# Kernel tuning notes

Measured on AMD Instinct MI355X. Metric: run time of the kernel, lower is better.

Reference implementation:

```python
import jax, jax.numpy as jnp
import numpy as np

N, MAXDEG, D = 100000, 16, 128
HID, OUT, BLOCKS, NUM_GRAPHS = 256, 1, 5, 2048
BN_EPS = 1e-5


def setup_inputs() -> dict:
    key = jax.random.key(0)
    ks = jax.random.split(key, 10)
    s = 0.05  # small init scale for stability across 5 residual blocks
    x = jax.random.normal(ks[0], (N, D), jnp.float32)
    nbr = jax.random.randint(ks[1], (N, MAXDEG), 0, N)
    pad_mask = jax.random.uniform(ks[2], (N, MAXDEG)) < 0.2
    padded_neighbors = jnp.where(pad_mask, -1, nbr)
    membership = jnp.sort(jax.random.randint(ks[3], (N,), 0, NUM_GRAPHS))
    return dict(
        x=x,
        padded_neighbors=padded_neighbors,
        membership=membership,
        merge_W=jax.random.normal(ks[4], (BLOCKS, 2 * D, D), jnp.float32) * s,
        merge_b=jnp.zeros((BLOCKS, D), jnp.float32),
        lin1_W=jax.random.normal(ks[5], (BLOCKS, D, HID), jnp.float32) * s,
        lin1_b=jnp.zeros((BLOCKS, HID), jnp.float32),
        lin2_W=jax.random.normal(ks[6], (BLOCKS, HID, D), jnp.float32) * s,
        lin2_b=jnp.zeros((BLOCKS, D), jnp.float32),
        bn_g=jnp.ones((BLOCKS, D), jnp.float32),
        bn_b=jnp.zeros((BLOCKS, D), jnp.float32),
        eps=jnp.full((BLOCKS,), 0.1, jnp.float32),
        dense0_W=jax.random.normal(ks[7], (D * (BLOCKS + 1), HID), jnp.float32) * s,
        dense0_b=jnp.zeros((HID,), jnp.float32),
        dense1_W=jax.random.normal(ks[8], (HID, D), jnp.float32) * s,
        dense1_b=jnp.zeros((D,), jnp.float32),
        bn0_g=jnp.ones((D,), jnp.float32),
        bn0_b=jnp.zeros((D,), jnp.float32),
        dense2_W=jax.random.normal(ks[9], (D, OUT), jnp.float32) * s,
        dense2_b=jnp.zeros((OUT,), jnp.float32),
    )


def _bn(h, g, b):
    # BatchNorm1d in training mode: batch stats, biased variance
    m = h.mean(0)
    v = h.var(0)
    return g * (h - m) * jax.lax.rsqrt(v + BN_EPS) + b


def _forward(x, padded_neighbors, membership, merge_W, merge_b, lin1_W, lin1_b,
             lin2_W, lin2_b, bn_g, bn_b, eps, dense0_W, dense0_b, dense1_W,
             dense1_b, bn0_g, bn0_b, dense2_W, dense2_b):
    # map padding value -1 to dummy row index N (mirrors torch's x_with_dummy[-1])
    idx = jnp.where(padded_neighbors >= 0, padded_neighbors, N)  # (N, MAXDEG)
    h = x
    xs = [x]
    for i in range(BLOCKS):
        # 'sum' aggregation == spmm(unnormalized adj, h): padded gather + sum
        hw_sum = jnp.concatenate([h, jnp.zeros((1, D), h.dtype)], axis=0)
        s_aggr = hw_sum[idx].sum(axis=1)  # (N, D)
        hw_max = jnp.concatenate([h, h.min(axis=0, keepdims=True)], axis=0)
        m_aggr = hw_max[idx].max(axis=1)  # (N, D)
        # merge='cat' -> merge_layer
        z = jnp.concatenate([s_aggr, m_aggr], axis=1) @ merge_W[i] + merge_b[i]
        # self_connection + learned eps * x_org
        z = z + h + eps[i] * h
        # backbone: Linear->ReLU->Linear->ReLU->BatchNorm1d
        z = jax.nn.relu(z @ lin1_W[i] + lin1_b[i])
        z = jax.nn.relu(z @ lin2_W[i] + lin2_b[i])
        z = _bn(z, bn_g[i], bn_b[i])
        xs.append(z)
        h = h + z  # add_dense_connection=True
    cat = jnp.concatenate(xs, axis=1)  # (N, D*(BLOCKS+1))
    # readout_method='sum': graph-level scatter-sum over membership
    g = jax.ops.segment_sum(cat, membership, num_segments=NUM_GRAPHS)
    g = jax.nn.relu(g @ dense0_W + dense0_b)
    g = jax.nn.relu(g @ dense1_W + dense1_b)
    g = _bn(g, bn0_g, bn0_b)
    return g @ dense2_W + dense2_b  # (NUM_GRAPHS, OUT)


def reference(x, padded_neighbors, membership, merge_W, merge_b, lin1_W, lin1_b,
              lin2_W, lin2_b, bn_g, bn_b, eps, dense0_W, dense0_b, dense1_W,
              dense1_b, bn0_g, bn0_b, dense2_W, dense2_b):
    return _forward(x, padded_neighbors, membership, merge_W, merge_b, lin1_W,
                    lin1_b, lin2_W, lin2_b, bn_g, bn_b, eps, dense0_W, dense0_b,
                    dense1_W, dense1_b, bn0_g, bn0_b, dense2_W, dense2_b)
```

## Files before the change

kernel.cpp:

```cpp
#include <hip/hip_runtime.h>
#include <hip/hip_bf16.h>
#include <math.h>

#define N_NODES 100000
#define DD 128
#define MAXDEG 16
#define HIDW 256
#define NBLOCKS 5
#define NGRAPH 2048
#define CATW 768

typedef __attribute__((ext_vector_type(8))) short short8;
typedef __attribute__((ext_vector_type(4))) float f32x4;

__device__ __forceinline__ float b2f(ushort u) {
    union { unsigned int i; float f; } x; x.i = ((unsigned int)u) << 16; return x.f;
}
__device__ __forceinline__ ushort f2b(float f) {
    unsigned int x = __float_as_uint(f);
    unsigned int r = (x + 0x7fffu + ((x >> 16) & 1u)) >> 16;
    return (ushort)r;
}
__device__ __forceinline__ unsigned int encf(float f) {
    unsigned int b = __float_as_uint(f);
    return (b & 0x80000000u) ? ~b : (b | 0x80000000u);
}
__device__ __forceinline__ float decf(unsigned int e) {
    return __uint_as_float((e & 0x80000000u) ? (e & 0x7fffffffu) : ~e);
}

__global__ __launch_bounds__(256)
void k_init(const float* __restrict__ x, float* __restrict__ h, ushort* __restrict__ hb)
{
    size_t i = ((size_t)blockIdx.x * 256 + threadIdx.x) * 4;
    float4 v = *reinterpret_cast<const float4*>(x + i);
    *reinterpret_cast<float4*>(h + i) = v;
    ushort4 u;
    u.x = f2b(v.x); u.y = f2b(v.y); u.z = f2b(v.z); u.w = f2b(v.w);
    *reinterpret_cast<ushort4*>(hb + i) = u;
}

__global__ void k_setup(unsigned int* __restrict__ cmin, float* __restrict__ bnacc)
{
    int t = threadIdx.x;
    for (int i = t; i < 6 * DD; i += 256) cmin[i] = 0xFF800000u;
    for (int i = t; i < NBLOCKS * 2 * DD; i += 256) bnacc[i] = 0.f;
}

__global__ __launch_bounds__(256)
void k_convT(const float* __restrict__ src, ushort* __restrict__ dst, int K, int M, int total)
{
    int id = blockIdx.x * 256 + threadIdx.x;
    if (id >= total) return;
    int km = K * M;
    int b = id / km, rem = id - b * km;
    int m = rem / K, k = rem - m * K;
    dst[(size_t)b * km + (size_t)m * K + k] = f2b(src[(size_t)b * km + (size_t)k * M + m]);
}

__global__ __launch_bounds__(256)
void k_colmin_part(const float* __restrict__ h, float* __restrict__ part, int nrows)
{
    int t = threadIdx.x;
    int c = t & 127, half = t >> 7;
    int r0 = blockIdx.x * 256;
    int rend = r0 + 256; if (rend > nrows) rend = nrows;
    float m = INFINITY;
    for (int r = r0 + half; r < rend; r += 2)
        m = fminf(m, h[(size_t)r * DD + c]);
    __shared__ float sm[256];
    sm[t] = m;
    __syncthreads();
    if (half == 0) part[(size_t)blockIdx.x * DD + c] = fminf(sm[c], sm[c + 128]);
}

__global__ void k_colmin_fin(const float* __restrict__ part, unsigned int* __restrict__ colmin, int nb)
{
    int c = threadIdx.x;
    float m = INFINITY;
    for (int b = 0; b < nb; ++b) m = fminf(m, part[(size_t)b * DD + c]);
    colmin[c] = encf(m);
}

__global__ __launch_bounds__(256)
void k_aggregate_b(const ushort* __restrict__ hb, const int* __restrict__ nbr,
                   const unsigned int* __restrict__ cmin, ushort* __restrict__ A)
{
    int t = threadIdx.x;
    int node = blockIdx.x * 8 + (t >> 5);
    int c0 = (t & 31) * 4;
    const int* row = nbr + (size_t)node * MAXDEG;
    float s0 = 0.f, s1 = 0.f, s2 = 0.f, s3 = 0.f;
    float m0 = -INFINITY, m1 = -INFINITY, m2 = -INFINITY, m3 = -INFINITY;
    int cnt = 0;
#pragma unroll
    for (int j = 0; j < MAXDEG; ++j) {
        int id = row[j];
        if (id >= 0) {
            uint2 v = *reinterpret_cast<const uint2*>(hb + (size_t)id * DD + c0);
            float f0 = __uint_as_float(v.x << 16);
            float f1 = __uint_as_float(v.x & 0xffff0000u);
            float f2 = __uint_as_float(v.y << 16);
            float f3 = __uint_as_float(v.y & 0xffff0000u);
            s0 += f0; s1 += f1; s2 += f2; s3 += f3;
            m0 = fmaxf(m0, f0); m1 = fmaxf(m1, f1);
            m2 = fmaxf(m2, f2); m3 = fmaxf(m3, f3);
            ++cnt;
        }
    }
    if (cnt == 0) {
        m0 = decf(cmin[c0]); m1 = decf(cmin[c0 + 1]);
        m2 = decf(cmin[c0 + 2]); m3 = decf(cmin[c0 + 3]);
    }
    ushort4 us, um;
    us.x = f2b(s0); us.y = f2b(s1); us.z = f2b(s2); us.w = f2b(s3);
    um.x = f2b(m0); um.y = f2b(m1); um.z = f2b(m2); um.w = f2b(m3);
    *reinterpret_cast<ushort4*>(A + (size_t)node * (2 * DD) + c0) = us;
    *reinterpret_cast<ushort4*>(A + (size_t)node * (2 * DD) + DD + c0) = um;
}

__global__ __launch_bounds__(256, 2)
void k_fused_mlp(const ushort* __restrict__ Ag, const float* __restrict__ h,
                 const ushort* __restrict__ mW, const ushort* __restrict__ w1,
                 const ushort* __restrict__ w2, const float* __restrict__ mb,
                 const float* __restrict__ b1, const float* __restrict__ b2,
                 const float* __restrict__ eps_ptr, float* __restrict__ uf,
                 float* __restrict__ bnacc)
{
    __shared__ __align__(16) char pool[72 * 1024];
    char* As = pool;
    char* Bs = pool + 8 * 1024;
    char* Zs = pool + 24 * 1024;
    char* Ts = pool + 40 * 1024;
    float* s1 = reinterpret_cast<float*>(pool);
    float* s2 = reinterpret_cast<float*>(pool) + 128;

    const int t = threadIdx.x;
    const int lane = t & 63, wave = t >> 6;
    const int wr = wave >> 1, wc = wave & 1;
    const int lr = lane & 15;
    const int lkb = (lane >> 4) << 4;
    const int rb = blockIdx.x * 64;

    f32x4 acc[2][4];
#pragma unroll
    for (int m = 0; m < 2; ++m)
#pragma unroll
        for (int n = 0; n < 4; ++n) acc[m][n] = (f32x4)(0.f);

    for (int k0 = 0; k0 < 256; k0 += 64) {
#pragma unroll
        for (int p = 0; p < 2; ++p) {
            int idx = p * 256 + t, row = idx >> 3, ch = idx & 7;
            int gr = rb + row;
            short8 v = {};
            if (gr < N_NODES)
                v = *reinterpret_cast<const short8*>(Ag + (size_t)gr * 256 + k0 + ch * 8);
            int byte = (row << 7) | (ch << 4); byte ^= (row & 7) << 4;
            *reinterpret_cast<short8*>(As + byte) = v;
        }
#pragma unroll
        for (int p = 0; p < 4; ++p) {
            int idx = p * 256 + t, row = idx >> 3, ch = idx & 7;
            short8 v = *reinterpret_cast<const short8*>(mW + (size_t)row * 256 + k0 + ch * 8);
            int byte = (row << 7) | (ch << 4); byte ^= (row & 7) << 4;
            *reinterpret_cast<short8*>(Bs + byte) = v;
        }
        __syncthreads();
#pragma unroll
        for (int k32 = 0; k32 < 2; ++k32) {
            short8 af[2], bq[4];
#pragma unroll
            for (int m = 0; m < 2; ++m) {
                int row = wr * 32 + m * 16 + lr;
                int byte = (row << 7) | (k32 * 64 + lkb); byte ^= (row & 7) << 4;
                af[m] = *reinterpret_cast<const short8*>(As + byte);
            }
#pragma unroll
            for (int n = 0; n < 4; ++n) {
                int col = wc * 64 + n * 16 + lr;
                int byte = (col << 7) | (k32 * 64 + lkb); byte ^= (col & 7) << 4;
                bq[n] = *reinterpret_cast<const short8*>(Bs + byte);
            }
#pragma unroll
            for (int m = 0; m < 2; ++m)
#pragma unroll
                for (int n = 0; n < 4; ++n)
                    acc[m][n] = __builtin_amdgcn_mfma_f32_16x16x32_bf16(af[m], bq[n], acc[m][n], 0, 0, 0);
        }
        __syncthreads();
    }
    {
        float alpha = 1.f + *eps_ptr;
#pragma unroll
        for (int m = 0; m < 2; ++m)
#pragma unroll
            for (int j = 0; j < 4; ++j) {
                int lrow = wr * 32 + m * 16 + (lane >> 4) * 4 + j;
                int grow = rb + lrow;
#pragma unroll
                for (int n = 0; n < 4; ++n) {
                    int col = wc * 64 + n * 16 + lr;
                    float z = acc[m][n][j] + mb[col];
                    if (grow < N_NODES) z += alpha * h[(size_t)grow * DD + col];
                    int byte = (lrow << 8) | (col << 1); byte ^= (lrow & 7) << 4;
                    *reinterpret_cast<ushort*>(Zs + byte) = f2b(z);
                }
            }
    }
    __syncthreads();

    f32x4 acb[2][8];
#pragma unroll
    for (int m = 0; m < 2; ++m)
#pragma unroll
        for (int n = 0; n < 8; ++n) acb[m][n] = (f32x4)(0.f);

    for (int kc = 0; kc < 4; ++kc) {
#pragma unroll
        for (int p = 0; p < 4; ++p) {
            int idx = p * 256 + t, row = idx >> 2, ch = idx & 3;
            short8 v = *reinterpret_cast<const short8*>(w1 + (size_t)row * 128 + kc * 32 + ch * 8);
            int byte = (row << 6) | (ch << 4); byte ^= (row & 3) << 4;
            *reinterpret_cast<short8*>(Bs + byte) = v;
        }
        __syncthreads();
        short8 af[2];
#pragma unroll
        for (int m = 0; m < 2; ++m) {
            int row = wr * 32 + m * 16 + lr;
            int byte = (row << 8) | (kc * 64 + lkb); byte ^= (row & 7) << 4;
            af[m] = *reinterpret_cast<const short8*>(Zs + byte);
        }
#pragma unroll
        for (int nh = 0; nh < 2; ++nh) {
            short8 bq[4];
#pragma unroll
            for (int q = 0; q < 4; ++q) {
                int wrow = wc * 128 + nh * 64 + q * 16 + lr;
                int byte = (wrow << 6) | lkb; byte ^= (wrow & 3) << 4;
                bq[q] = *reinterpret_cast<const short8*>(Bs + byte);
            }
#pragma unroll
            for (int m = 0; m < 2; ++m)
#pragma unroll
                for (int q = 0; q < 4; ++q)
                    acb[m][nh * 4 + q] = __builtin_amdgcn_mfma_f32_16x16x32_bf16(af[m], bq[q], acb[m][nh * 4 + q], 0, 0, 0);
        }
        __syncthreads();
    }
    {
#pragma unroll
        for (int m = 0; m < 2; ++m)
#pragma unroll
            for (int j = 0; j < 4; ++j) {
                int lrow = wr * 32 + m * 16 + (lane >> 4) * 4 + j;
#pragma unroll
                for (int nn = 0; nn < 8; ++nn) {
                    int col = wc * 128 + nn * 16 + lr;
                    float tv = fmaxf(acb[m][nn][j] + b1[col], 0.f);
                    int byte = (lrow << 9) | (col << 1); byte ^= (lrow & 7) << 4;
                    *reinterpret_cast<ushort*>(Ts + byte) = f2b(tv);
                }
            }
    }
    __syncthreads();

    f32x4 acu[2][4];
#pragma unroll
    for (int m = 0; m < 2; ++m)
#pragma unroll
        for (int n = 0; n < 4; ++n) acu[m][n] = (f32x4)(0.f);

    for (int k0 = 0; k0 < 256; k0 += 64) {
#pragma unroll
        for (int p = 0; p < 4; ++p) {
            int idx = p * 256 + t, row = idx >> 3, ch = idx & 7;
            short8 v = *reinterpret_cast<const short8*>(w2 + (size_t)row * 256 + k0 + ch * 8);
            int byte = (row << 7) | (ch << 4); byte ^= (row & 7) << 4;
            *reinterpret_cast<short8*>(Bs + byte) = v;
        }
        __syncthreads();
#pragma unroll
        for (int k32 = 0; k32 < 2; ++k32) {
            short8 af[2], bq[4];
#pragma unroll
            for (int m = 0; m < 2; ++m) {
                int row = wr * 32 + m * 16 + lr;
                int byte = (row << 9) | (k0 * 2 + k32 * 64 + lkb); byte ^= (row & 7) << 4;
                af[m] = *reinterpret_cast<const short8*>(Ts + byte);
            }
#pragma unroll
            for (int n = 0; n < 4; ++n) {
                int wrow = wc * 64 + n * 16 + lr;
                int byte = (wrow << 7) | (k32 * 64 + lkb); byte ^= (wrow & 7) << 4;
                bq[n] = *reinterpret_cast<const short8*>(Bs + byte);
            }
#pragma unroll
            for (int m = 0; m < 2; ++m)
#pragma unroll
                for (int n = 0; n < 4; ++n)
                    acu[m][n] = __builtin_amdgcn_mfma_f32_16x16x32_bf16(af[m], bq[n], acu[m][n], 0, 0, 0);
        }
        __syncthreads();
    }
    if (t < 128) { s1[t] = 0.f; s2[t] = 0.f; }
    __syncthreads();
    {
        float e1[4] = {0.f, 0.f, 0.f, 0.f}, e2[4] = {0.f, 0.f, 0.f, 0.f};
#pragma unroll
        for (int m = 0; m < 2; ++m)
#pragma unroll
            for (int j = 0; j < 4; ++j) {
                int grow = rb + wr * 32 + m * 16 + (lane >> 4) * 4 + j;
                if (grow >= N_NODES) continue;
#pragma unroll
                for (int n = 0; n < 4; ++n) {
                    int col = wc * 64 + n * 16 + lr;
                    float u = fmaxf(acu[m][n][j] + b2[col], 0.f);
                    uf[(size_t)grow * DD + col] = u;
                    e1[n] += u; e2[n] += u * u;
                }
            }
#pragma unroll
        for (int n = 0; n < 4; ++n) {
            int col = wc * 64 + n * 16 + lr;
            atomicAdd(&s1[col], e1[n]);
            atomicAdd(&s2[col], e2[n]);
        }
    }
    __syncthreads();
    if (t < 128) {
        atomicAdd(&bnacc[t], s1[t]);
        atomicAdd(&bnacc[128 + t], s2[t]);
    }
}

__global__ void k_bn_fin(const float* __restrict__ part, int nb, float inv_n,
                         float* __restrict__ mean, float* __restrict__ inv)
{
    int c = threadIdx.x;
    float s1 = 0.f, s2 = 0.f;
    for (int b = 0; b < nb; ++b) {
        s1 += part[(size_t)b * 256 + c];
        s2 += part[(size_t)b * 256 + 128 + c];
    }
    float m = s1 * inv_n;
    float v = s2 * inv_n - m * m;
    mean[c] = m;
    inv[c] = rsqrtf(v + 1e-5f);
}

__global__ __launch_bounds__(256)
void k_bn_apply_scan(const float* __restrict__ u, float* __restrict__ h,
                     ushort* __restrict__ hb,
                     const float* __restrict__ mean, const float* __restrict__ inv,
                     const float* __restrict__ gam, const float* __restrict__ bet,
                     const int* __restrict__ mem, float* __restrict__ G,
                     unsigned int* __restrict__ cmin_next,
                     int colbase, int nrows)
{
    int t = threadIdx.x;
    int c = t & 127, half = t >> 7;
    int r0 = blockIdx.x * 128;
    int rend = r0 + 128; if (rend > nrows) rend = nrows;
    float mu = mean[c], iv = inv[c], g = gam[c], b = bet[c];
    float accv = 0.f, lmin = INFINITY;
    int curg = -1;
    for (int r = r0 + half; r < rend; r += 2) {
        float z = g * (u[(size_t)r * DD + c] - mu) * iv + b;
        float hn = h[(size_t)r * DD + c] + z;
        h[(size_t)r * DD + c] = hn;
        hb[(size_t)r * DD + c] = f2b(hn);
        lmin = fminf(lmin, hn);
        int gg = mem[r];
        if (gg != curg) {
            if (curg >= 0) atomicAdd(&G[(size_t)curg * CATW + colbase + c], accv);
            curg = gg; accv = 0.f;
        }
        accv += z;
    }
    if (curg >= 0) atomicAdd(&G[(size_t)curg * CATW + colbase + c], accv);
    __shared__ float sm[256];
    sm[t] = lmin;
    __syncthreads();
    if (half == 0) atomicMin(&cmin_next[c], encf(fminf(sm[c], sm[c + 128])));
}

__global__ __launch_bounds__(256)
void k_scan_x(const float* __restrict__ x, const int* __restrict__ mem,
              float* __restrict__ G, int nrows)
{
    int t = threadIdx.x;
    int c = t & 127, half = t >> 7;
    int r0 = blockIdx.x * 128;
    int rend = r0 + 128; if (rend > nrows) rend = nrows;
    float accv = 0.f;
    int curg = -1;
    for (int r = r0 + half; r < rend; r += 2) {
        float z = x[(size_t)r * DD + c];
        int gg = mem[r];
        if (gg != curg) {
            if (curg >= 0) atomicAdd(&G[(size_t)curg * CATW + c], accv);
            curg = gg; accv = 0.f;
        }
        accv += z;
    }
    if (curg >= 0) atomicAdd(&G[(size_t)curg * CATW + c], accv);
}

__global__ __launch_bounds__(256)
void k_bn_part(const float* __restrict__ u, float* __restrict__ part, int nrows)
{
    int t = threadIdx.x;
    int c = t & 127, half = t >> 7;
    int r0 = blockIdx.x * 256;
    int rend = r0 + 256; if (rend > nrows) rend = nrows;
    float s1 = 0.f, s2 = 0.f;
    for (int r = r0 + half; r < rend; r += 2) {
        float v = u[(size_t)r * DD + c];
        s1 += v; s2 += v * v;
    }
    __shared__ float sh1[256], sh2[256];
    sh1[t] = s1; sh2[t] = s2;
    __syncthreads();
    if (half == 0) {
        part[(size_t)blockIdx.x * 256 + c]       = sh1[c] + sh1[c + 128];
        part[(size_t)blockIdx.x * 256 + 128 + c] = sh2[c] + sh2[c + 128];
    }
}

__global__ __launch_bounds__(256)
void k_read0(const float* __restrict__ G, const float* __restrict__ W,
             const float* __restrict__ b, float* __restrict__ o)
{
    __shared__ float As[8][CATW];
    int t = threadIdx.x;
    int rb = blockIdx.x * 8;
#pragma unroll
    for (int p = 0; p < 6; ++p) {
        int idx = p * 256 + t;
        int r = idx / 192, k4 = idx - r * 192;
        float4 v = *reinterpret_cast<const float4*>(G + (size_t)(rb + r) * CATW + k4 * 4);
        *reinterpret_cast<float4*>(&As[r][k4 * 4]) = v;
    }
    __syncthreads();
    float acc[8] = {0.f, 0.f, 0.f, 0.f, 0.f, 0.f, 0.f, 0.f};
    for (int k = 0; k < CATW; k += 4) {
        float w0 = W[(size_t)(k + 0) * HIDW + t];
        float w1 = W[(size_t)(k + 1) * HIDW + t];
        float w2 = W[(size_t)(k + 2) * HIDW + t];
        float w3 = W[(size_t)(k + 3) * HIDW + t];
#pragma unroll
        for (int r = 0; r < 8; ++r) {
            float4 a = *reinterpret_cast<const float4*>(&As[r][k]);
            acc[r] += a.x * w0 + a.y * w1 + a.z * w2 + a.w * w3;
        }
    }
    float bb = b[t];
#pragma unroll
    for (int r = 0; r < 8; ++r)
        o[(size_t)(rb + r) * HIDW + t] = fmaxf(acc[r] + bb, 0.f);
}

__global__ __launch_bounds__(256)
void k_read1(const float* __restrict__ A, const float* __restrict__ W,
             const float* __restrict__ b, float* __restrict__ o)
{
    __shared__ float As[16][HIDW];
    int t = threadIdx.x;
    int c = t & 127, rh = t >> 7;
    int rb = blockIdx.x * 16;
#pragma unroll
    for (int p = 0; p < 4; ++p) {
        int idx = p * 256 + t;
        int r = idx >> 6, k4 = idx & 63;
        float4 v = *reinterpret_cast<const float4*>(A + (size_t)(rb + r) * HIDW + k4 * 4);
        *reinterpret_cast<float4*>(&As[r][k4 * 4]) = v;
    }
    __syncthreads();
    float acc[8] = {0.f, 0.f, 0.f, 0.f, 0.f, 0.f, 0.f, 0.f};
    for (int k = 0; k < HIDW; k += 4) {
        float w0 = W[(size_t)(k + 0) * DD + c];
        float w1 = W[(size_t)(k + 1) * DD + c];
        float w2 = W[(size_t)(k + 2) * DD + c];
        float w3 = W[(size_t)(k + 3) * DD + c];
#pragma unroll
        for (int r = 0; r < 8; ++r) {
            float4 a = *reinterpret_cast<const float4*>(&As[rh * 8 + r][k]);
            acc[r] += a.x * w0 + a.y * w1 + a.z * w2 + a.w * w3;
        }
    }
    float bb = b[c];
#pragma unroll
    for (int r = 0; r < 8; ++r)
        o[(size_t)(rb + rh * 8 + r) * DD + c] = fmaxf(acc[r] + bb, 0.f);
}

__global__ __launch_bounds__(256)
void k_final(const float* __restrict__ g1, const float* __restrict__ mean,
             const float* __restrict__ inv, const float* __restrict__ gam,
             const float* __restrict__ bet, const float* __restrict__ W2,
             const float* __restrict__ b2, float* __restrict__ out)
{
    int w = threadIdx.x >> 6, lane = threadIdx.x & 63;
    int row = blockIdx.x * 4 + w;
    float s = 0.f;
#pragma unroll
    for (int q = 0; q < 2; ++q) {
        int c = lane + q * 64;
        float v = gam[c] * (g1[(size_t)row * DD + c] - mean[c]) * inv[c] + bet[c];
        s += v * W2[c];
    }
#pragma unroll
    for (int off = 32; off > 0; off >>= 1) s += __shfl_down(s, off);
    if (lane == 0) out[row] = s + b2[0];
}

extern "C" void kernel_launch(void* const* d_in, const int* in_sizes, int n_in,
                              void* d_out, int out_size, void* d_ws, size_t ws_size,
                              hipStream_t stream)
{
    const float* x       = (const float*)d_in[0];
    const int*   nbr     = (const int*)d_in[1];
    const int*   mem     = (const int*)d_in[2];
    const float* merge_W = (const float*)d_in[3];
    const float* merge_b = (const float*)d_in[4];
    const float* lin1_W  = (const float*)d_in[5];
    const float* lin1_b  = (const float*)d_in[6];
    const float* lin2_W  = (const float*)d_in[7];
    const float* lin2_b  = (const float*)d_in[8];
    const float* bn_g    = (const float*)d_in[9];
    const float* bn_b    = (const float*)d_in[10];
    const float* epsv    = (const float*)d_in[11];
    const float* d0W     = (const float*)d_in[12];
    const float* d0b     = (const float*)d_in[13];
    const float* d1W     = (const float*)d_in[14];
    const float* d1b     = (const float*)d_in[15];
    const float* bn0g    = (const float*)d_in[16];
    const float* bn0b    = (const float*)d_in[17];
    const float* d2W     = (const float*)d_in[18];
    const float* d2b     = (const float*)d_in[19];
    float* out = (float*)d_out;

    char* p = (char*)d_ws;
    auto alloc = [&](size_t bytes) { char* r = p; p += (bytes + 255) & ~(size_t)255; return r; };
    float*  h     = (float*)alloc((size_t)N_NODES * DD * 4);
    ushort* hb    = (ushort*)alloc((size_t)N_NODES * DD * 2);
    ushort* Abuf  = (ushort*)alloc((size_t)N_NODES * 2 * DD * 2);
    float*  uf    = (float*)alloc((size_t)N_NODES * DD * 4);
    float*  G     = (float*)alloc((size_t)NGRAPH * CATW * 4);
    float*  g0    = (float*)alloc((size_t)NGRAPH * HIDW * 4);
    float*  g1    = (float*)alloc((size_t)NGRAPH * DD * 4);
    float*  part  = (float*)alloc((size_t)391 * 256 * 4);
    float*  red   = (float*)alloc(1024 * 4);
    unsigned int* cminb = (unsigned int*)alloc(6 * DD * 4);
    float*  bnacc = (float*)alloc((size_t)NBLOCKS * 2 * DD * 4);
    ushort* mergeT = (ushort*)alloc((size_t)NBLOCKS * 2 * DD * DD * 2);
    ushort* lin1T  = (ushort*)alloc((size_t)NBLOCKS * DD * HIDW * 2);
    ushort* lin2T  = (ushort*)alloc((size_t)NBLOCKS * HIDW * DD * 2);
    float* meanp  = red + DD;
    float* invp   = red + 2 * DD;

    const int NBP = 391;
    const int NRB = 782;
    const int NFB = 1563;

    k_init<<<12500, 256, 0, stream>>>(x, h, hb);
    k_setup<<<1, 256, 0, stream>>>(cminb, bnacc);
    {
        int tm = NBLOCKS * 2 * DD * DD;
        k_convT<<<(tm + 255) / 256, 256, 0, stream>>>(merge_W, mergeT, 2 * DD, DD, tm);
        int t1 = NBLOCKS * DD * HIDW;
        k_convT<<<(t1 + 255) / 256, 256, 0, stream>>>(lin1_W, lin1T, DD, HIDW, t1);
        int t2 = NBLOCKS * HIDW * DD;
        k_convT<<<(t2 + 255) / 256, 256, 0, stream>>>(lin2_W, lin2T, HIDW, DD, t2);
    }
    hipMemsetAsync(G, 0, (size_t)NGRAPH * CATW * sizeof(float), stream);
    k_colmin_part<<<NBP, 256, 0, stream>>>(x, part, N_NODES);
    k_colmin_fin<<<1, 128, 0, stream>>>(part, cminb, NBP);
    k_scan_x<<<NRB, 256, 0, stream>>>(x, mem, G, N_NODES);

    for (int i = 0; i < NBLOCKS; ++i) {
        k_aggregate_b<<<N_NODES / 8, 256, 0, stream>>>(hb, nbr, cminb + (size_t)i * DD, Abuf);
        k_fused_mlp<<<NFB, 256, 0, stream>>>(
            Abuf, h,
            mergeT + (size_t)i * 2 * DD * DD,
            lin1T + (size_t)i * DD * HIDW,
            lin2T + (size_t)i * HIDW * DD,
            merge_b + (size_t)i * DD, lin1_b + (size_t)i * HIDW, lin2_b + (size_t)i * DD,
            epsv + i, uf, bnacc + (size_t)i * 2 * DD);
        k_bn_fin<<<1, 128, 0, stream>>>(bnacc + (size_t)i * 2 * DD, 1, 1.f / (float)N_NODES, meanp, invp);
        k_bn_apply_scan<<<NRB, 256, 0, stream>>>(uf, h, hb, meanp, invp,
                                                 bn_g + (size_t)i * DD, bn_b + (size_t)i * DD,
                                                 mem, G, cminb + (size_t)(i + 1) * DD,
                                                 (i + 1) * DD, N_NODES);
    }

    k_read0<<<NGRAPH / 8, 256, 0, stream>>>(G, d0W, d0b, g0);
    k_read1<<<NGRAPH / 16, 256, 0, stream>>>(g0, d1W, d1b, g1);
    k_bn_part<<<8, 256, 0, stream>>>(g1, part, NGRAPH);
    k_bn_fin<<<1, 128, 0, stream>>>(part, 8, 1.f / (float)NGRAPH, meanp, invp);
    k_final<<<NGRAPH / 4, 256, 0, stream>>>(g1, meanp, invp, bn0g, bn0b, d2W, d2b, out);
}
```

Baseline: 1.617 ms.

## Restructure fused MLP to per-wave row tiles with direct global weight fragments

Replaces the block-cooperative fused MLP, which staged A and weight tiles through LDS with many __syncthreads, with a kernel where each wave owns 32 rows. Each wave loads MFMA operand fragments for A and weights straight from global memory, using L2 for weight reuse. The hidden layer is processed in 32-column chunks so lin1 output feeds lin2 through a small per-wave LDS buffer without block barriers. BN statistics are reduced with wave shuffles before global atomics, and the aggregate kernel is widened to 8 columns per thread with 16-byte loads. The risk is higher global and L2 traffic for weights, since they are no longer shared across waves through LDS.

```diff
diff --git a/kernel.cpp b/kernel.cpp
--- a/kernel.cpp
+++ b/kernel.cpp
@@ -87,252 +87,193 @@
                    const unsigned int* __restrict__ cmin, ushort* __restrict__ A)
 {
     int t = threadIdx.x;
-    int node = blockIdx.x * 8 + (t >> 5);
-    int c0 = (t & 31) * 4;
+    int node = blockIdx.x * 16 + (t >> 4);
+    int c0 = (t & 15) * 8;
     const int* row = nbr + (size_t)node * MAXDEG;
-    float s0 = 0.f, s1 = 0.f, s2 = 0.f, s3 = 0.f;
-    float m0 = -INFINITY, m1 = -INFINITY, m2 = -INFINITY, m3 = -INFINITY;
+    float s[8], mx[8];
+#pragma unroll
+    for (int q = 0; q < 8; ++q) { s[q] = 0.f; mx[q] = -INFINITY; }
     int cnt = 0;
 #pragma unroll
     for (int j = 0; j < MAXDEG; ++j) {
         int id = row[j];
         if (id >= 0) {
-            uint2 v = *reinterpret_cast<const uint2*>(hb + (size_t)id * DD + c0);
-            float f0 = __uint_as_float(v.x << 16);
-            float f1 = __uint_as_float(v.x & 0xffff0000u);
-            float f2 = __uint_as_float(v.y << 16);
-            float f3 = __uint_as_float(v.y & 0xffff0000u);
-            s0 += f0; s1 += f1; s2 += f2; s3 += f3;
-            m0 = fmaxf(m0, f0); m1 = fmaxf(m1, f1);
-            m2 = fmaxf(m2, f2); m3 = fmaxf(m3, f3);
+            uint4 v = *reinterpret_cast<const uint4*>(hb + (size_t)id * DD + c0);
+            unsigned int w0 = v.x, w1 = v.y, w2 = v.z, w3 = v.w;
+            float f0 = __uint_as_float(w0 << 16),  f1 = __uint_as_float(w0 & 0xffff0000u);
+            float f2 = __uint_as_float(w1 << 16),  f3 = __uint_as_float(w1 & 0xffff0000u);
+            float f4 = __uint_as_float(w2 << 16),  f5 = __uint_as_float(w2 & 0xffff0000u);
+            float f6 = __uint_as_float(w3 << 16),  f7 = __uint_as_float(w3 & 0xffff0000u);
+            s[0] += f0; s[1] += f1; s[2] += f2; s[3] += f3;
+            s[4] += f4; s[5] += f5; s[6] += f6; s[7] += f7;
+            mx[0] = fmaxf(mx[0], f0); mx[1] = fmaxf(mx[1], f1);
+            mx[2] = fmaxf(mx[2], f2); mx[3] = fmaxf(mx[3], f3);
+            mx[4] = fmaxf(mx[4], f4); mx[5] = fmaxf(mx[5], f5);
+            mx[6] = fmaxf(mx[6], f6); mx[7] = fmaxf(mx[7], f7);
             ++cnt;
         }
     }
     if (cnt == 0) {
-        m0 = decf(cmin[c0]); m1 = decf(cmin[c0 + 1]);
-        m2 = decf(cmin[c0 + 2]); m3 = decf(cmin[c0 + 3]);
-    }
-    ushort4 us, um;
-    us.x = f2b(s0); us.y = f2b(s1); us.z = f2b(s2); us.w = f2b(s3);
-    um.x = f2b(m0); um.y = f2b(m1); um.z = f2b(m2); um.w = f2b(m3);
-    *reinterpret_cast<ushort4*>(A + (size_t)node * (2 * DD) + c0) = us;
-    *reinterpret_cast<ushort4*>(A + (size_t)node * (2 * DD) + DD + c0) = um;
-}
-
-__global__ __launch_bounds__(256, 2)
-void k_fused_mlp(const ushort* __restrict__ Ag, const float* __restrict__ h,
-                 const ushort* __restrict__ mW, const ushort* __restrict__ w1,
-                 const ushort* __restrict__ w2, const float* __restrict__ mb,
-                 const float* __restrict__ b1, const float* __restrict__ b2,
-                 const float* __restrict__ eps_ptr, float* __restrict__ uf,
-                 float* __restrict__ bnacc)
-{
-    __shared__ __align__(16) char pool[72 * 1024];
-    char* As = pool;
-    char* Bs = pool + 8 * 1024;
-    char* Zs = pool + 24 * 1024;
-    char* Ts = pool + 40 * 1024;
-    float* s1 = reinterpret_cast<float*>(pool);
-    float* s2 = reinterpret_cast<float*>(pool) + 128;
-
+#pragma unroll
+        for (int q = 0; q < 8; ++q) mx[q] = decf(cmin[c0 + q]);
+    }
+    short8 vs, vm;
+#pragma unroll
+    for (int q = 0; q < 8; ++q) { vs[q] = (short)f2b(s[q]); vm[q] = (short)f2b(mx[q]); }
+    *reinterpret_cast<short8*>(A + (size_t)node * (2 * DD) + c0) = vs;
+    *reinterpret_cast<short8*>(A + (size_t)node * (2 * DD) + DD + c0) = vm;
+}
+
+__global__ __launch_bounds__(256)
+void k_fused_wave(const ushort* __restrict__ Ag, const float* __restrict__ h,
+                  const ushort* __restrict__ mW, const ushort* __restrict__ w1,
+                  const ushort* __restrict__ w2, const float* __restrict__ mb,
+                  const float* __restrict__ b1, const float* __restrict__ b2,
+                  const float* __restrict__ eps_ptr, float* __restrict__ uf,
+                  float* __restrict__ bnacc)
+{
+    __shared__ __align__(16) char pool[40960];
     const int t = threadIdx.x;
     const int lane = t & 63, wave = t >> 6;
-    const int wr = wave >> 1, wc = wave & 1;
+    char* zs = pool + wave * 10240;
+    char* ts = zs + 8192;
     const int lr = lane & 15;
-    const int lkb = (lane >> 4) << 4;
-    const int rb = blockIdx.x * 64;
-
-    f32x4 acc[2][4];
+    const int lg = lane >> 4;
+    const int r0 = blockIdx.x * 128 + wave * 32;
+    const float alpha = 1.f + *eps_ptr;
+
+    f32x4 acc[2][8];
 #pragma unroll
     for (int m = 0; m < 2; ++m)
 #pragma unroll
-        for (int n = 0; n < 4; ++n) acc[m][n] = (f32x4)(0.f);
-
-    for (int k0 = 0; k0 < 256; k0 += 64) {
-#pragma unroll
-        for (int p = 0; p < 2; ++p) {
-            int idx = p * 256 + t, row = idx >> 3, ch = idx & 7;
-            int gr = rb + row;
-            short8 v = {};
-            if (gr < N_NODES)
-                v = *reinterpret_cast<const short8*>(Ag + (size_t)gr * 256 + k0 + ch * 8);
-            int byte = (row << 7) | (ch << 4); byte ^= (row & 7) << 4;
-            *reinterpret_cast<short8*>(As + byte) = v;
-        }
-#pragma unroll
-        for (int p = 0; p < 4; ++p) {
-            int idx = p * 256 + t, row = idx >> 3, ch = idx & 7;
-            short8 v = *reinterpret_cast<const short8*>(mW + (size_t)row * 256 + k0 + ch * 8);
-            int byte = (row << 7) | (ch << 4); byte ^= (row & 7) << 4;
-            *reinterpret_cast<short8*>(Bs + byte) = v;
-        }
-        __syncthreads();
-#pragma unroll
-        for (int k32 = 0; k32 < 2; ++k32) {
-            short8 af[2], bq[4];
+        for (int n = 0; n < 8; ++n) acc[m][n] = (f32x4)(0.f);
+
+    const ushort* agp = Ag + (size_t)(r0 + lr) * 256 + lg * 8;
+    const ushort* mwp = mW + (size_t)lr * 256 + lg * 8;
+    const bool ok0 = (r0 + lr) < N_NODES;
+    const bool ok1 = (r0 + 16 + lr) < N_NODES;
+#pragma unroll 2
+    for (int k32 = 0; k32 < 8; ++k32) {
+        short8 af0 = {}, af1 = {};
+        if (ok0) af0 = *reinterpret_cast<const short8*>(agp + k32 * 32);
+        if (ok1) af1 = *reinterpret_cast<const short8*>(agp + 16 * 256 + k32 * 32);
+#pragma unroll
+        for (int n = 0; n < 8; ++n) {
+            short8 bq = *reinterpret_cast<const short8*>(mwp + (size_t)n * 16 * 256 + k32 * 32);
+            acc[0][n] = __builtin_amdgcn_mfma_f32_16x16x32_bf16(af0, bq, acc[0][n], 0, 0, 0);
+            acc[1][n] = __builtin_amdgcn_mfma_f32_16x16x32_bf16(af1, bq, acc[1][n], 0, 0, 0);
+        }
+    }
+#pragma unroll
+    for (int m = 0; m < 2; ++m)
+#pragma unroll
+        for (int j = 0; j < 4; ++j) {
+            int lrow = m * 16 + lg * 4 + j;
+            int grow = r0 + lrow;
+#pragma unroll
+            for (int n = 0; n < 8; ++n) {
+                int col = n * 16 + lr;
+                float z = acc[m][n][j] + mb[col];
+                if (grow < N_NODES) z += alpha * h[(size_t)grow * DD + col];
+                int byte = (lrow << 8) | (col << 1);
+                byte ^= (lrow & 7) << 4;
+                *reinterpret_cast<ushort*>(zs + byte) = f2b(z);
+            }
+        }
+    asm volatile("s_waitcnt lgkmcnt(0)" ::: "memory");
+    __builtin_amdgcn_sched_barrier(0);
+
+    f32x4 au[2][8];
+#pragma unroll
+    for (int m = 0; m < 2; ++m)
+#pragma unroll
+        for (int n = 0; n < 8; ++n) au[m][n] = (f32x4)(0.f);
+
+    const ushort* w1p = w1 + (size_t)lr * 128 + lg * 8;
+    const ushort* w2p = w2 + (size_t)lr * 256 + lg * 8;
+    for (int hc = 0; hc < 8; ++hc) {
+        f32x4 at[2][2];
+#pragma unroll
+        for (int m = 0; m < 2; ++m)
+#pragma unroll
+            for (int n2 = 0; n2 < 2; ++n2) at[m][n2] = (f32x4)(0.f);
+#pragma unroll
+        for (int k32 = 0; k32 < 4; ++k32) {
+            short8 az[2];
 #pragma unroll
             for (int m = 0; m < 2; ++m) {
-                int row = wr * 32 + m * 16 + lr;
-                int byte = (row << 7) | (k32 * 64 + lkb); byte ^= (row & 7) << 4;
-                af[m] = *reinterpret_cast<const short8*>(As + byte);
+                int row = m * 16 + lr;
+                int byte = (row << 8) | (k32 << 6) | (lg << 4);
+                byte ^= (lr & 7) << 4;
+                az[m] = *reinterpret_cast<const short8*>(zs + byte);
             }
 #pragma unroll
-            for (int n = 0; n < 4; ++n) {
-                int col = wc * 64 + n * 16 + lr;
-                int byte = (col << 7) | (k32 * 64 + lkb); byte ^= (col & 7) << 4;
-                bq[n] = *reinterpret_cast<const short8*>(Bs + byte);
+            for (int n2 = 0; n2 < 2; ++n2) {
+                short8 bq = *reinterpret_cast<const short8*>(
+                    w1p + (size_t)(hc * 32 + n2 * 16) * 128 + k32 * 32);
+                at[0][n2] = __builtin_amdgcn_mfma_f32_16x16x32_bf16(az[0], bq, at[0][n2], 0, 0, 0);
+                at[1][n2] = __builtin_amdgcn_mfma_f32_16x16x32_bf16(az[1], bq, at[1][n2], 0, 0, 0);
             }
-#pragma unroll
-            for (int m = 0; m < 2; ++m)
-#pragma unroll
-                for (int n = 0; n < 4; ++n)
-                    acc[m][n] = __builtin_amdgcn_mfma_f32_16x16x32_bf16(af[m], bq[n], acc[m][n], 0, 0, 0);
-        }
-        __syncthreads();
-    }
-    {
-        float alpha = 1.f + *eps_ptr;
+        }
 #pragma unroll
         for (int m = 0; m < 2; ++m)
 #pragma unroll
             for (int j = 0; j < 4; ++j) {
-                int lrow = wr * 32 + m * 16 + (lane >> 4) * 4 + j;
-                int grow = rb + lrow;
-#pragma unroll
-                for (int n = 0; n < 4; ++n) {
-                    int col = wc * 64 + n * 16 + lr;
-                    float z = acc[m][n][j] + mb[col];
-                    if (grow < N_NODES) z += alpha * h[(size_t)grow * DD + col];
-                    int byte = (lrow << 8) | (col << 1); byte ^= (lrow & 7) << 4;
-                    *reinterpret_cast<ushort*>(Zs + byte) = f2b(z);
+                int lrow = m * 16 + lg * 4 + j;
+#pragma unroll
+                for (int n2 = 0; n2 < 2; ++n2) {
+                    int hcol = n2 * 16 + lr;
+                    float tv = fmaxf(at[m][n2][j] + b1[hc * 32 + hcol], 0.f);
+                    int byte = (lrow << 6) | (hcol << 1);
+                    byte ^= (lrow & 3) << 4;
+                    *reinterpret_cast<ushort*>(ts + byte) = f2b(tv);
                 }
             }
-    }
-    __syncthreads();
-
-    f32x4 acb[2][8];
+        asm volatile("s_waitcnt lgkmcnt(0)" ::: "memory");
+        __builtin_amdgcn_sched_barrier(0);
+        short8 atf[2];
+#pragma unroll
+        for (int m = 0; m < 2; ++m) {
+            int row = m * 16 + lr;
+            int byte = (row << 6) | (lg << 4);
+            byte ^= (lr & 3) << 4;
+            atf[m] = *reinterpret_cast<const short8*>(ts + byte);
+        }
+#pragma unroll
+        for (int n = 0; n < 8; ++n) {
+            short8 bq = *reinterpret_cast<const short8*>(
+                w2p + (size_t)n * 16 * 256 + hc * 32);
+            au[0][n] = __builtin_amdgcn_mfma_f32_16x16x32_bf16(atf[0], bq, au[0][n], 0, 0, 0);
+            au[1][n] = __builtin_amdgcn_mfma_f32_16x16x32_bf16(atf[1], bq, au[1][n], 0, 0, 0);
+        }
+    }
+
+    float e1[8], e2[8];
+#pragma unroll
+    for (int n = 0; n < 8; ++n) { e1[n] = 0.f; e2[n] = 0.f; }
 #pragma unroll
     for (int m = 0; m < 2; ++m)
 #pragma unroll
-        for (int n = 0; n < 8; ++n) acb[m][n] = (f32x4)(0.f);
-
-    for (int kc = 0; kc < 4; ++kc) {
-#pragma unroll
-        for (int p = 0; p < 4; ++p) {
-            int idx = p * 256 + t, row = idx >> 2, ch = idx & 3;
-            short8 v = *reinterpret_cast<const short8*>(w1 + (size_t)row * 128 + kc * 32 + ch * 8);
-            int byte = (row << 6) | (ch << 4); byte ^= (row & 3) << 4;
-            *reinterpret_cast<short8*>(Bs + byte) = v;
-        }
-        __syncthreads();
-        short8 af[2];
-#pragma unroll
-        for (int m = 0; m < 2; ++m) {
-            int row = wr * 32 + m * 16 + lr;
-            int byte = (row << 8) | (kc * 64 + lkb); byte ^= (row & 7) << 4;
-            af[m] = *reinterpret_cast<const short8*>(Zs + byte);
-        }
-#pragma unroll
-        for (int nh = 0; nh < 2; ++nh) {
-            short8 bq[4];
-#pragma unroll
-            for (int q = 0; q < 4; ++q) {
-                int wrow = wc * 128 + nh * 64 + q * 16 + lr;
-                int byte = (wrow << 6) | lkb; byte ^= (wrow & 3) << 4;
-                bq[q] = *reinterpret_cast<const short8*>(Bs + byte);
+        for (int j = 0; j < 4; ++j) {
+            int grow = r0 + m * 16 + lg * 4 + j;
+            if (grow >= N_NODES) continue;
+#pragma unroll
+            for (int n = 0; n < 8; ++n) {
+                int col = n * 16 + lr;
+                float u = fmaxf(au[m][n][j] + b2[col], 0.f);
+                uf[(size_t)grow * DD + col] = u;
+                e1[n] += u; e2[n] += u * u;
             }
-#pragma unroll
-            for (int m = 0; m < 2; ++m)
-#pragma unroll
-                for (int q = 0; q < 4; ++q)
-                    acb[m][nh * 4 + q] = __builtin_amdgcn_mfma_f32_16x16x32_bf16(af[m], bq[q], acb[m][nh * 4 + q], 0, 0, 0);
-        }
-        __syncthreads();
-    }
-    {
-#pragma unroll
-        for (int m = 0; m < 2; ++m)
-#pragma unroll
-            for (int j = 0; j < 4; ++j) {
-                int lrow = wr * 32 + m * 16 + (lane >> 4) * 4 + j;
-#pragma unroll
-                for (int nn = 0; nn < 8; ++nn) {
-                    int col = wc * 128 + nn * 16 + lr;
-                    float tv = fmaxf(acb[m][nn][j] + b1[col], 0.f);
-                    int byte = (lrow << 9) | (col << 1); byte ^= (lrow & 7) << 4;
-                    *reinterpret_cast<ushort*>(Ts + byte) = f2b(tv);
-                }
-            }
-    }
-    __syncthreads();
-
-    f32x4 acu[2][4];
-#pragma unroll
-    for (int m = 0; m < 2; ++m)
-#pragma unroll
-        for (int n = 0; n < 4; ++n) acu[m][n] = (f32x4)(0.f);
-
-    for (int k0 = 0; k0 < 256; k0 += 64) {
-#pragma unroll
-        for (int p = 0; p < 4; ++p) {
-            int idx = p * 256 + t, row = idx >> 3, ch = idx & 7;
-            short8 v = *reinterpret_cast<const short8*>(w2 + (size_t)row * 256 + k0 + ch * 8);
-            int byte = (row << 7) | (ch << 4); byte ^= (row & 7) << 4;
-            *reinterpret_cast<short8*>(Bs + byte) = v;
-        }
-        __syncthreads();
-#pragma unroll
-        for (int k32 = 0; k32 < 2; ++k32) {
-            short8 af[2], bq[4];
-#pragma unroll
-            for (int m = 0; m < 2; ++m) {
-                int row = wr * 32 + m * 16 + lr;
-                int byte = (row << 9) | (k0 * 2 + k32 * 64 + lkb); byte ^= (row & 7) << 4;
-                af[m] = *reinterpret_cast<const short8*>(Ts + byte);
-            }
-#pragma unroll
-            for (int n = 0; n < 4; ++n) {
-                int wrow = wc * 64 + n * 16 + lr;
-                int byte = (wrow << 7) | (k32 * 64 + lkb); byte ^= (wrow & 7) << 4;
-                bq[n] = *reinterpret_cast<const short8*>(Bs + byte);
-            }
-#pragma unroll
-            for (int m = 0; m < 2; ++m)
-#pragma unroll
-                for (int n = 0; n < 4; ++n)
-                    acu[m][n] = __builtin_amdgcn_mfma_f32_16x16x32_bf16(af[m], bq[n], acu[m][n], 0, 0, 0);
-        }
-        __syncthreads();
-    }
-    if (t < 128) { s1[t] = 0.f; s2[t] = 0.f; }
-    __syncthreads();
-    {
-        float e1[4] = {0.f, 0.f, 0.f, 0.f}, e2[4] = {0.f, 0.f, 0.f, 0.f};
-#pragma unroll
-        for (int m = 0; m < 2; ++m)
-#pragma unroll
-            for (int j = 0; j < 4; ++j) {
-                int grow = rb + wr * 32 + m * 16 + (lane >> 4) * 4 + j;
-                if (grow >= N_NODES) continue;
-#pragma unroll
-                for (int n = 0; n < 4; ++n) {
-                    int col = wc * 64 + n * 16 + lr;
-                    float u = fmaxf(acu[m][n][j] + b2[col], 0.f);
-                    uf[(size_t)grow * DD + col] = u;
-                    e1[n] += u; e2[n] += u * u;
-                }
-            }
-#pragma unroll
-        for (int n = 0; n < 4; ++n) {
-            int col = wc * 64 + n * 16 + lr;
-            atomicAdd(&s1[col], e1[n]);
-            atomicAdd(&s2[col], e2[n]);
-        }
-    }
-    __syncthreads();
-    if (t < 128) {
-        atomicAdd(&bnacc[t], s1[t]);
-        atomicAdd(&bnacc[128 + t], s2[t]);
+        }
+#pragma unroll
+    for (int n = 0; n < 8; ++n) {
+        float a = e1[n], b = e2[n];
+        a += __shfl_xor(a, 16); b += __shfl_xor(b, 16);
+        a += __shfl_xor(a, 32); b += __shfl_xor(b, 32);
+        if (lg == 0) {
+            atomicAdd(&bnacc[n * 16 + lr], a);
+            atomicAdd(&bnacc[128 + n * 16 + lr], b);
+        }
     }
 }
 
@@ -564,7 +505,6 @@
 
     const int NBP = 391;
     const int NRB = 782;
-    const int NFB = 1563;
 
     k_init<<<12500, 256, 0, stream>>>(x, h, hb);
     k_setup<<<1, 256, 0, stream>>>(cminb, bnacc);
@@ -582,8 +522,8 @@
     k_scan_x<<<NRB, 256, 0, stream>>>(x, mem, G, N_NODES);
 
     for (int i = 0; i < NBLOCKS; ++i) {
-        k_aggregate_b<<<N_NODES / 8, 256, 0, stream>>>(hb, nbr, cminb + (size_t)i * DD, Abuf);
-        k_fused_mlp<<<NFB, 256, 0, stream>>>(
+        k_aggregate_b<<<N_NODES / 16, 256, 0, stream>>>(hb, nbr, cminb + (size_t)i * DD, Abuf);
+        k_fused_wave<<<NRB, 256, 0, stream>>>(
             Abuf, h,
             mergeT + (size_t)i * 2 * DD * DD,
             lin1T + (size_t)i * DD * HIDW,
```

Measured after the change: 1.794 ms. 11.0% more time.

## Restructure fused MLP to stream hidden chunks and widen aggregate loads

Applied to the files above, without the earlier changes.

The fused MLP kernel now interleaves lin1 and lin2 per 64-wide hidden chunk, so the full 64x256 hidden tile no longer has to sit in shared memory. This cuts LDS from 72KB to 48KB and raises the launch-bounds occupancy hint from 2 to 3 blocks. Warps are re-tiled so each wave owns all 64 rows and a column slice, and the BN statistics are reduced with wave shuffles and global atomics instead of shared-memory atomics. The aggregate kernel gathers 8 bf16 per thread with 16-byte loads and handles 16 nodes per block; the per-chunk lin1 step adds extra barriers, and the higher occupancy target may pressure registers.

```diff
diff --git a/kernel.cpp b/kernel.cpp
--- a/kernel.cpp
+++ b/kernel.cpp
@@ -87,39 +87,44 @@
                    const unsigned int* __restrict__ cmin, ushort* __restrict__ A)
 {
     int t = threadIdx.x;
-    int node = blockIdx.x * 8 + (t >> 5);
-    int c0 = (t & 31) * 4;
+    int node = blockIdx.x * 16 + (t >> 4);
+    int c0 = (t & 15) * 8;
     const int* row = nbr + (size_t)node * MAXDEG;
-    float s0 = 0.f, s1 = 0.f, s2 = 0.f, s3 = 0.f;
-    float m0 = -INFINITY, m1 = -INFINITY, m2 = -INFINITY, m3 = -INFINITY;
+    float s[8], mx[8];
+#pragma unroll
+    for (int q = 0; q < 8; ++q) { s[q] = 0.f; mx[q] = -INFINITY; }
     int cnt = 0;
 #pragma unroll
     for (int j = 0; j < MAXDEG; ++j) {
         int id = row[j];
         if (id >= 0) {
-            uint2 v = *reinterpret_cast<const uint2*>(hb + (size_t)id * DD + c0);
-            float f0 = __uint_as_float(v.x << 16);
-            float f1 = __uint_as_float(v.x & 0xffff0000u);
-            float f2 = __uint_as_float(v.y << 16);
-            float f3 = __uint_as_float(v.y & 0xffff0000u);
-            s0 += f0; s1 += f1; s2 += f2; s3 += f3;
-            m0 = fmaxf(m0, f0); m1 = fmaxf(m1, f1);
-            m2 = fmaxf(m2, f2); m3 = fmaxf(m3, f3);
+            uint4 v = *reinterpret_cast<const uint4*>(hb + (size_t)id * DD + c0);
+            unsigned int w0 = v.x, w1 = v.y, w2 = v.z, w3 = v.w;
+            float f0 = __uint_as_float(w0 << 16),  f1 = __uint_as_float(w0 & 0xffff0000u);
+            float f2 = __uint_as_float(w1 << 16),  f3 = __uint_as_float(w1 & 0xffff0000u);
+            float f4 = __uint_as_float(w2 << 16),  f5 = __uint_as_float(w2 & 0xffff0000u);
+            float f6 = __uint_as_float(w3 << 16),  f7 = __uint_as_float(w3 & 0xffff0000u);
+            s[0] += f0; s[1] += f1; s[2] += f2; s[3] += f3;
+            s[4] += f4; s[5] += f5; s[6] += f6; s[7] += f7;
+            mx[0] = fmaxf(mx[0], f0); mx[1] = fmaxf(mx[1], f1);
+            mx[2] = fmaxf(mx[2], f2); mx[3] = fmaxf(mx[3], f3);
+            mx[4] = fmaxf(mx[4], f4); mx[5] = fmaxf(mx[5], f5);
+            mx[6] = fmaxf(mx[6], f6); mx[7] = fmaxf(mx[7], f7);
             ++cnt;
         }
     }
     if (cnt == 0) {
-        m0 = decf(cmin[c0]); m1 = decf(cmin[c0 + 1]);
-        m2 = decf(cmin[c0 + 2]); m3 = decf(cmin[c0 + 3]);
-    }
-    ushort4 us, um;
-    us.x = f2b(s0); us.y = f2b(s1); us.z = f2b(s2); us.w = f2b(s3);
-    um.x = f2b(m0); um.y = f2b(m1); um.z = f2b(m2); um.w = f2b(m3);
-    *reinterpret_cast<ushort4*>(A + (size_t)node * (2 * DD) + c0) = us;
-    *reinterpret_cast<ushort4*>(A + (size_t)node * (2 * DD) + DD + c0) = um;
-}
-
-__global__ __launch_bounds__(256, 2)
+#pragma unroll
+        for (int q = 0; q < 8; ++q) mx[q] = decf(cmin[c0 + q]);
+    }
+    short8 vs, vm;
+#pragma unroll
+    for (int q = 0; q < 8; ++q) { vs[q] = (short)f2b(s[q]); vm[q] = (short)f2b(mx[q]); }
+    *reinterpret_cast<short8*>(A + (size_t)node * (2 * DD) + c0) = vs;
+    *reinterpret_cast<short8*>(A + (size_t)node * (2 * DD) + DD + c0) = vm;
+}
+
+__global__ __launch_bounds__(256, 3)
 void k_fused_mlp(const ushort* __restrict__ Ag, const float* __restrict__ h,
                  const ushort* __restrict__ mW, const ushort* __restrict__ w1,
                  const ushort* __restrict__ w2, const float* __restrict__ mb,
@@ -127,26 +132,25 @@
                  const float* __restrict__ eps_ptr, float* __restrict__ uf,
                  float* __restrict__ bnacc)
 {
-    __shared__ __align__(16) char pool[72 * 1024];
+    __shared__ __align__(16) char pool[48 * 1024];
     char* As = pool;
     char* Bs = pool + 8 * 1024;
     char* Zs = pool + 24 * 1024;
     char* Ts = pool + 40 * 1024;
-    float* s1 = reinterpret_cast<float*>(pool);
-    float* s2 = reinterpret_cast<float*>(pool) + 128;
 
     const int t = threadIdx.x;
     const int lane = t & 63, wave = t >> 6;
-    const int wr = wave >> 1, wc = wave & 1;
     const int lr = lane & 15;
-    const int lkb = (lane >> 4) << 4;
+    const int lg = lane >> 4;
+    const int lkb = lg << 4;
     const int rb = blockIdx.x * 64;
-
-    f32x4 acc[2][4];
-#pragma unroll
-    for (int m = 0; m < 2; ++m)
-#pragma unroll
-        for (int n = 0; n < 4; ++n) acc[m][n] = (f32x4)(0.f);
+    const float alpha = 1.f + *eps_ptr;
+
+    f32x4 acc[4][2];
+#pragma unroll
+    for (int m = 0; m < 4; ++m)
+#pragma unroll
+        for (int n = 0; n < 2; ++n) acc[m][n] = (f32x4)(0.f);
 
     for (int k0 = 0; k0 < 256; k0 += 64) {
 #pragma unroll
@@ -169,38 +173,37 @@
         __syncthreads();
 #pragma unroll
         for (int k32 = 0; k32 < 2; ++k32) {
-            short8 af[2], bq[4];
-#pragma unroll
-            for (int m = 0; m < 2; ++m) {
-                int row = wr * 32 + m * 16 + lr;
+            short8 af[4], bq[2];
+#pragma unroll
+            for (int m = 0; m < 4; ++m) {
+                int row = m * 16 + lr;
                 int byte = (row << 7) | (k32 * 64 + lkb); byte ^= (row & 7) << 4;
                 af[m] = *reinterpret_cast<const short8*>(As + byte);
             }
 #pragma unroll
-            for (int n = 0; n < 4; ++n) {
-                int col = wc * 64 + n * 16 + lr;
+            for (int n = 0; n < 2; ++n) {
+                int col = wave * 32 + n * 16 + lr;
                 int byte = (col << 7) | (k32 * 64 + lkb); byte ^= (col & 7) << 4;
                 bq[n] = *reinterpret_cast<const short8*>(Bs + byte);
             }
 #pragma unroll
-            for (int m = 0; m < 2; ++m)
-#pragma unroll
-                for (int n = 0; n < 4; ++n)
+            for (int m = 0; m < 4; ++m)
+#pragma unroll
+                for (int n = 0; n < 2; ++n)
                     acc[m][n] = __builtin_amdgcn_mfma_f32_16x16x32_bf16(af[m], bq[n], acc[m][n], 0, 0, 0);
         }
         __syncthreads();
     }
     {
-        float alpha = 1.f + *eps_ptr;
-#pragma unroll
-        for (int m = 0; m < 2; ++m)
+#pragma unroll
+        for (int m = 0; m < 4; ++m)
 #pragma unroll
             for (int j = 0; j < 4; ++j) {
-                int lrow = wr * 32 + m * 16 + (lane >> 4) * 4 + j;
+                int lrow = m * 16 + lg * 4 + j;
                 int grow = rb + lrow;
 #pragma unroll
-                for (int n = 0; n < 4; ++n) {
-                    int col = wc * 64 + n * 16 + lr;
+                for (int n = 0; n < 2; ++n) {
+                    int col = wave * 32 + n * 16 + lr;
                     float z = acc[m][n][j] + mb[col];
                     if (grow < N_NODES) z += alpha * h[(size_t)grow * DD + col];
                     int byte = (lrow << 8) | (col << 1); byte ^= (lrow & 7) << 4;
@@ -210,129 +213,105 @@
     }
     __syncthreads();
 
-    f32x4 acb[2][8];
-#pragma unroll
-    for (int m = 0; m < 2; ++m)
-#pragma unroll
-        for (int n = 0; n < 8; ++n) acb[m][n] = (f32x4)(0.f);
-
-    for (int kc = 0; kc < 4; ++kc) {
+    f32x4 au[4][2];
+#pragma unroll
+    for (int m = 0; m < 4; ++m)
+#pragma unroll
+        for (int n = 0; n < 2; ++n) au[m][n] = (f32x4)(0.f);
+
+    for (int hc = 0; hc < 4; ++hc) {
 #pragma unroll
         for (int p = 0; p < 4; ++p) {
-            int idx = p * 256 + t, row = idx >> 2, ch = idx & 3;
-            short8 v = *reinterpret_cast<const short8*>(w1 + (size_t)row * 128 + kc * 32 + ch * 8);
-            int byte = (row << 6) | (ch << 4); byte ^= (row & 3) << 4;
+            int idx = p * 256 + t, row = idx >> 4, ch = idx & 15;
+            short8 v = *reinterpret_cast<const short8*>(w1 + (size_t)(hc * 64 + row) * 128 + ch * 8);
+            int byte = (row << 8) | (ch << 4); byte ^= (row & 7) << 4;
             *reinterpret_cast<short8*>(Bs + byte) = v;
         }
         __syncthreads();
-        short8 af[2];
-#pragma unroll
-        for (int m = 0; m < 2; ++m) {
-            int row = wr * 32 + m * 16 + lr;
-            int byte = (row << 8) | (kc * 64 + lkb); byte ^= (row & 7) << 4;
-            af[m] = *reinterpret_cast<const short8*>(Zs + byte);
-        }
-#pragma unroll
-        for (int nh = 0; nh < 2; ++nh) {
-            short8 bq[4];
-#pragma unroll
-            for (int q = 0; q < 4; ++q) {
-                int wrow = wc * 128 + nh * 64 + q * 16 + lr;
-                int byte = (wrow << 6) | lkb; byte ^= (wrow & 3) << 4;
-                bq[q] = *reinterpret_cast<const short8*>(Bs + byte);
-            }
-#pragma unroll
-            for (int m = 0; m < 2; ++m)
-#pragma unroll
-                for (int q = 0; q < 4; ++q)
-                    acb[m][nh * 4 + q] = __builtin_amdgcn_mfma_f32_16x16x32_bf16(af[m], bq[q], acb[m][nh * 4 + q], 0, 0, 0);
-        }
+        f32x4 at[4];
+#pragma unroll
+        for (int m = 0; m < 4; ++m) at[m] = (f32x4)(0.f);
+#pragma unroll
+        for (int kc = 0; kc < 4; ++kc) {
+            int wrow = wave * 16 + lr;
+            int bbyte = (wrow << 8) | (kc * 64 + lkb); bbyte ^= (wrow & 7) << 4;
+            short8 bq = *reinterpret_cast<const short8*>(Bs + bbyte);
+#pragma unroll
+            for (int m = 0; m < 4; ++m) {
+                int row = m * 16 + lr;
+                int byte = (row << 8) | (kc * 64 + lkb); byte ^= (row & 7) << 4;
+                short8 az = *reinterpret_cast<const short8*>(Zs + byte);
+                at[m] = __builtin_amdgcn_mfma_f32_16x16x32_bf16(az, bq, at[m], 0, 0, 0);
+            }
+        }
+#pragma unroll
+        for (int m = 0; m < 4; ++m)
+#pragma unroll
+            for (int j = 0; j < 4; ++j) {
+                int lrow = m * 16 + lg * 4 + j;
+                int hidc = wave * 16 + lr;
+                float tv = fmaxf(at[m][j] + b1[hc * 64 + hidc], 0.f);
+                int byte = (lrow << 7) | (hidc << 1); byte ^= (lrow & 7) << 4;
+                *reinterpret_cast<ushort*>(Ts + byte) = f2b(tv);
+            }
         __syncthreads();
-    }
-    {
-#pragma unroll
-        for (int m = 0; m < 2; ++m)
-#pragma unroll
-            for (int j = 0; j < 4; ++j) {
-                int lrow = wr * 32 + m * 16 + (lane >> 4) * 4 + j;
-#pragma unroll
-                for (int nn = 0; nn < 8; ++nn) {
-                    int col = wc * 128 + nn * 16 + lr;
-                    float tv = fmaxf(acb[m][nn][j] + b1[col], 0.f);
-                    int byte = (lrow << 9) | (col << 1); byte ^= (lrow & 7) << 4;
-                    *reinterpret_cast<ushort*>(Ts + byte) = f2b(tv);
-                }
-            }
-    }
-    __syncthreads();
-
-    f32x4 acu[2][4];
-#pragma unroll
-    for (int m = 0; m < 2; ++m)
-#pragma unroll
-        for (int n = 0; n < 4; ++n) acu[m][n] = (f32x4)(0.f);
-
-    for (int k0 = 0; k0 < 256; k0 += 64) {
 #pragma unroll
         for (int p = 0; p < 4; ++p) {
             int idx = p * 256 + t, row = idx >> 3, ch = idx & 7;
-            short8 v = *reinterpret_cast<const short8*>(w2 + (size_t)row * 256 + k0 + ch * 8);
+            short8 v = *reinterpret_cast<const short8*>(w2 + (size_t)row * 256 + hc * 64 + ch * 8);
             int byte = (row << 7) | (ch << 4); byte ^= (row & 7) << 4;
             *reinterpret_cast<short8*>(Bs + byte) = v;
         }
         __syncthreads();
 #pragma unroll
         for (int k32 = 0; k32 < 2; ++k32) {
-            short8 af[2], bq[4];
-#pragma unroll
-            for (int m = 0; m < 2; ++m) {
-                int row = wr * 32 + m * 16 + lr;
-                int byte = (row << 9) | (k0 * 2 + k32 * 64 + lkb); byte ^= (row & 7) << 4;
-                af[m] = *reinterpret_cast<const short8*>(Ts + byte);
-            }
-#pragma unroll
-            for (int n = 0; n < 4; ++n) {
-                int wrow = wc * 64 + n * 16 + lr;
+            short8 atf[4], bq[2];
+#pragma unroll
+            for (int m = 0; m < 4; ++m) {
+                int row = m * 16 + lr;
+                int byte = (row << 7) | (k32 * 64 + lkb); byte ^= (row & 7) << 4;
+                atf[m] = *reinterpret_cast<const short8*>(Ts + byte);
+            }
+#pragma unroll
+            for (int n = 0; n < 2; ++n) {
+                int wrow = wave * 32 + n * 16 + lr;
                 int byte = (wrow << 7) | (k32 * 64 + lkb); byte ^= (wrow & 7) << 4;
                 bq[n] = *reinterpret_cast<const short8*>(Bs + byte);
             }
 #pragma unroll
-            for (int m = 0; m < 2; ++m)
-#pragma unroll
-                for (int n = 0; n < 4; ++n)
-                    acu[m][n] = __builtin_amdgcn_mfma_f32_16x16x32_bf16(af[m], bq[n], acu[m][n], 0, 0, 0);
+            for (int m = 0; m < 4; ++m)
+#pragma unroll
+                for (int n = 0; n < 2; ++n)
+                    au[m][n] = __builtin_amdgcn_mfma_f32_16x16x32_bf16(atf[m], bq[n], au[m][n], 0, 0, 0);
         }
         __syncthreads();
     }
-    if (t < 128) { s1[t] = 0.f; s2[t] = 0.f; }
-    __syncthreads();
-    {
-        float e1[4] = {0.f, 0.f, 0.f, 0.f}, e2[4] = {0.f, 0.f, 0.f, 0.f};
-#pragma unroll
-        for (int m = 0; m < 2; ++m)
-#pragma unroll
-            for (int j = 0; j < 4; ++j) {
-                int grow = rb + wr * 32 + m * 16 + (lane >> 4) * 4 + j;
-                if (grow >= N_NODES) continue;
-#pragma unroll
-                for (int n = 0; n < 4; ++n) {
-                    int col = wc * 64 + n * 16 + lr;
-                    float u = fmaxf(acu[m][n][j] + b2[col], 0.f);
-                    uf[(size_t)grow * DD + col] = u;
-                    e1[n] += u; e2[n] += u * u;
-                }
-            }
-#pragma unroll
-        for (int n = 0; n < 4; ++n) {
-            int col = wc * 64 + n * 16 + lr;
-            atomicAdd(&s1[col], e1[n]);
-            atomicAdd(&s2[col], e2[n]);
-        }
-    }
-    __syncthreads();
-    if (t < 128) {
-        atomicAdd(&bnacc[t], s1[t]);
-        atomicAdd(&bnacc[128 + t], s2[t]);
+
+    float e1[2] = {0.f, 0.f}, e2[2] = {0.f, 0.f};
+#pragma unroll
+    for (int m = 0; m < 4; ++m)
+#pragma unroll
+        for (int j = 0; j < 4; ++j) {
+            int grow = rb + m * 16 + lg * 4 + j;
+            if (grow >= N_NODES) continue;
+#pragma unroll
+            for (int n = 0; n < 2; ++n) {
+                int col = wave * 32 + n * 16 + lr;
+                float u = fmaxf(au[m][n][j] + b2[col], 0.f);
+                uf[(size_t)grow * DD + col] = u;
+                e1[n] += u; e2[n] += u * u;
+            }
+        }
+#pragma unroll
+    for (int n = 0; n < 2; ++n) {
+        int col = wave * 32 + n * 16 + lr;
+        float a = e1[n], b = e2[n];
+        a += __shfl_xor(a, 16); b += __shfl_xor(b, 16);
+        a += __shfl_xor(a, 32); b += __shfl_xor(b, 32);
+        if (lg == 0) {
+            atomicAdd(&bnacc[col], a);
+            atomicAdd(&bnacc[128 + col], b);
+        }
     }
 }
 
@@ -582,7 +561,7 @@
     k_scan_x<<<NRB, 256, 0, stream>>>(x, mem, G, N_NODES);
 
     for (int i = 0; i < NBLOCKS; ++i) {
-        k_aggregate_b<<<N_NODES / 8, 256, 0, stream>>>(hb, nbr, cminb + (size_t)i * DD, Abuf);
+        k_aggregate_b<<<N_NODES / 16, 256, 0, stream>>>(hb, nbr, cminb + (size_t)i * DD, Abuf);
         k_fused_mlp<<<NFB, 256, 0, stream>>>(
             Abuf, h,
             mergeT + (size_t)i * 2 * DD * DD,
```

Result: faster. 1.328 ms (-17.9%).
